# Kernel optimization log

Hardware: AMD Instinct MI355X
Metric: run time of the kernel (lower is better)

The kernel has to match this reference:

```python
import jax, jax.numpy as jnp
import numpy as np

B = 262144
MA = [128, 128]
MB = [128, 128]


def krone_linear(x_a, x_b, wa, wb, ba, bb):
    # slice inputs to each branch's in_features (torch slices the wider branch)
    ia, ib = wa.shape[1], wb.shape[1]
    x_a = x_a[:, :ia]
    x_b = x_b[:, :ib]
    h_a = x_a @ wa.T + ba
    h_b = x_b @ wb.T + bb
    # zero-pad the narrower output so both branches share a width (static shapes)
    oa, ob = wa.shape[0], wb.shape[0]
    if oa > ob:
        h_b = jnp.pad(h_b, ((0, 0), (0, oa - ob)))
    elif ob > oa:
        h_a = jnp.pad(h_a, ((0, 0), (0, ob - oa)))
    return h_a, h_b


def krone_softmax(x_a, x_b, fa, fb):
    x_a = x_a[:, :fa]
    x_b = x_b[:, :fb]
    # vectorized per-row Kronecker product: kron(a, b)[i*fb + j] = a[i]*b[j]
    y = (x_a[:, :, None] * x_b[:, None, :]).reshape(x_a.shape[0], fa * fb)
    return jax.nn.softmax(y, axis=1)


def setup_inputs() -> dict:
    key = jax.random.key(0)
    ks = jax.random.split(key, 13)
    s = 0.1
    inp = {
        "x": jax.random.normal(ks[0], (2, B, 2), dtype=jnp.float32),
        "w1a": jax.random.normal(ks[1], (MA[0], 2), dtype=jnp.float32) * s,
        "w1b": jax.random.normal(ks[2], (MB[0], 2), dtype=jnp.float32) * s,
        "b1a": jax.random.normal(ks[3], (MA[0],), dtype=jnp.float32) * s,
        "b1b": jax.random.normal(ks[4], (MB[0],), dtype=jnp.float32) * s,
        "w2a": jax.random.normal(ks[5], (MA[1], MA[0]), dtype=jnp.float32) * s,
        "w2b": jax.random.normal(ks[6], (MB[1], MB[0]), dtype=jnp.float32) * s,
        "b2a": jax.random.normal(ks[7], (MA[1],), dtype=jnp.float32) * s,
        "b2b": jax.random.normal(ks[8], (MB[1],), dtype=jnp.float32) * s,
        "w3a": jax.random.normal(ks[9], (1, MA[1]), dtype=jnp.float32) * s,
        "w3b": jax.random.normal(ks[10], (3, MB[1]), dtype=jnp.float32) * s,
        "b3a": jax.random.normal(ks[11], (1,), dtype=jnp.float32) * s,
        "b3b": jax.random.normal(ks[12], (3,), dtype=jnp.float32) * s,
    }
    return inp


def reference(x, w1a, w1b, b1a, b1b, w2a, w2b, b2a, b2b, w3a, w3b, b3a, b3b):
    x_a, x_b = x[0], x[1]
    h_a, h_b = krone_linear(x_a, x_b, w1a, w1b, b1a, b1b)
    h_a, h_b = jax.nn.relu(h_a), jax.nn.relu(h_b)
    h_a, h_b = krone_linear(h_a, h_b, w2a, w2b, b2a, b2b)
    h_a, h_b = jax.nn.relu(h_a), jax.nn.relu(h_b)
    h_a, h_b = krone_linear(h_a, h_b, w3a, w3b, b3a, b3b)
    return krone_softmax(h_a, h_b, 1, 3)
```

## Files before the change

kernel.cpp:

```cpp
#include <hip/hip_runtime.h>
#include <hip/hip_bf16.h>


#define BTOT 262144
#define NBLK (BTOT / 512)

typedef __attribute__((ext_vector_type(2))) float floatx2;
typedef __attribute__((ext_vector_type(4))) float floatx4;
typedef __attribute__((ext_vector_type(8))) short bf16x8;
typedef __attribute__((ext_vector_type(4))) int  intx4;

#define OFF_W2  0
#define OFF_W1  65536
#define OFF_B2  68608
#define OFF_W3A 69632
#define OFF_W3B 70144
#define OFF_SA  71680
#define LDS_TOTAL 73728

#if __has_builtin(__builtin_amdgcn_cvt_pk_bf16_f32)
static __device__ __forceinline__ int pack2bf(float lo, float hi) {
    return __builtin_bit_cast(int, __builtin_amdgcn_cvt_pk_bf16_f32(lo, hi));
}
#else
static __device__ __forceinline__ int pack2bf(float lo, float hi) {
    unsigned a = __builtin_bit_cast(unsigned, lo) + 0x8000u;
    unsigned b = __builtin_bit_cast(unsigned, hi) + 0x8000u;
    return (int)__builtin_amdgcn_perm(b, a, 0x07060302u);
}
#endif

#define SEL4(v, i) \
    ((i) == 0 ? (v).x : (i) == 1 ? (v).y : (i) == 2 ? (v).z : (v).w)

static __device__ __forceinline__ floatx4 redcol4(floatx4 v) {
    #pragma unroll
    for (int m = 1; m <= 8; m <<= 1) {
        floatx4 t;
        t.x = __shfl_xor(v.x, m);
        t.y = __shfl_xor(v.y, m);
        t.z = __shfl_xor(v.z, m);
        t.w = __shfl_xor(v.w, m);
        v = v + t;
    }
    return v;
}

static __device__ __forceinline__ floatx4 splat4(float s) {
    return (floatx4){s, s, s, s};
}

#define GEMM_CHUNK(acc, XV, W1P, W2p)                                          \
    {                                                                          \
        const floatx4 Z4 = (floatx4){0.f, 0.f, 0.f, 0.f};                      \
        _Pragma("unroll")                                                      \
        for (int s = 0; s < 4; ++s) {                                          \
            intx4 af[2];                                                       \
            _Pragma("unroll")                                                  \
            for (int j2 = 0; j2 < 4; ++j2) {                                   \
                int kp = s * 16 + quad * 4 + j2;                               \
                floatx2 w0p = (W1P)[kp * 3];                                   \
                floatx2 w1p = (W1P)[kp * 3 + 1];                               \
                floatx2 b1p = (W1P)[kp * 3 + 2];                               \
                _Pragma("unroll")                                              \
                for (int mt = 0; mt < 2; ++mt) {                               \
                    floatx2 xx = (floatx2){(XV)[mt].x, (XV)[mt].x};            \
                    floatx2 xy = (floatx2){(XV)[mt].y, (XV)[mt].y};            \
                    floatx2 h = __builtin_elementwise_fma(xx, w0p,             \
                                  __builtin_elementwise_fma(xy, w1p, b1p));    \
                    h = __builtin_elementwise_max(h, (floatx2){0.f, 0.f});     \
                    af[mt][j2] = pack2bf(h.x, h.y);                            \
                }                                                              \
            }                                                                  \
            _Pragma("unroll")                                                  \
            for (int t = 0; t < 8; ++t) {                                      \
                bf16x8 bfr = (W2p)[(s * 8 + t) * 64 + lane];                   \
                _Pragma("unroll")                                              \
                for (int mt = 0; mt < 2; ++mt) {                               \
                    if (s == 0)                                                \
                        acc[t][mt] = __builtin_amdgcn_mfma_f32_16x16x32_bf16(  \
                            __builtin_bit_cast(bf16x8, af[mt]), bfr, Z4,       \
                            0, 0, 0);                                          \
                    else                                                       \
                        acc[t][mt] = __builtin_amdgcn_mfma_f32_16x16x32_bf16(  \
                            __builtin_bit_cast(bf16x8, af[mt]), bfr,           \
                            acc[t][mt], 0, 0, 0);                              \
                }                                                              \
            }                                                                  \
        }                                                                      \
    }

__global__ __launch_bounds__(512, 4)
void krone_fused(const float* __restrict__ x,
                 const float* __restrict__ w1a, const float* __restrict__ w1b,
                 const float* __restrict__ b1a, const float* __restrict__ b1b,
                 const float* __restrict__ w2a, const float* __restrict__ w2b,
                 const float* __restrict__ b2a, const float* __restrict__ b2b,
                 const float* __restrict__ w3a, const float* __restrict__ w3b,
                 const float* __restrict__ b3a, const float* __restrict__ b3b,
                 float* __restrict__ out) {
    __shared__ __align__(16) unsigned char smem[LDS_TOTAL];

    const int tid  = threadIdx.x;
    const int lane = tid & 63;
    const int wave = tid >> 6;
    const int quad = lane >> 4;
    const int col  = lane & 15;
    const int wbase = blockIdx.x * 512 + wave * 64;

    {
        #pragma unroll
        for (int i = 0; i < 16; ++i) {
            const int path = i >> 3;
            const float4* w2p = (const float4*)(path ? w2b : w2a);
            int n  = (tid & 15) | ((i & 7) << 4);
            int k4 = tid >> 4;
            float4 f = w2p[n * 32 + k4];
            int k = k4 * 4;
            int s = k >> 5;
            int j0 = k & 7;
            int l = ((k & 31) >> 3) * 16 + (n & 15);
            int2 pkd;
            pkd.x = pack2bf(f.x, f.y);
            pkd.y = pack2bf(f.z, f.w);
            *(int2*)(smem + OFF_W2 + path * 32768 +
                     (s * 8 + (n >> 4)) * 1024 + l * 16 + j0 * 2) = pkd;
        }
        if (tid < 128) {
            int p = tid >> 6, kp = tid & 63;
            const float* w1 = p ? w1b : w1a;
            const float* b1 = p ? b1b : b1a;
            float4 w4 = ((const float4*)w1)[kp];
            floatx2* dst = (floatx2*)(smem + OFF_W1) + p * 192 + kp * 3;
            dst[0] = (floatx2){w4.x, w4.z};
            dst[1] = (floatx2){w4.y, w4.w};
            dst[2] = (floatx2){b1[2 * kp], b1[2 * kp + 1]};
            ((float*)(smem + OFF_B2))[tid] = b2a[tid];
            ((float*)(smem + OFF_W3A))[tid] = w3a[tid];
        } else if (tid < 256) {
            ((float*)(smem + OFF_B2))[tid] = b2b[tid - 128];
        }
        if (tid >= 128)
            ((float*)(smem + OFF_W3B))[tid - 128] = w3b[tid - 128];
    }

    const bf16x8*  W2A = (const bf16x8*)(smem + OFF_W2);
    const bf16x8*  W2B = (const bf16x8*)(smem + OFF_W2 + 32768);
    const floatx2* W1A = (const floatx2*)(smem + OFF_W1);
    const floatx2* W1B = W1A + 192;
    const float*   B2A = (const float*)(smem + OFF_B2);
    const float*   B2B = B2A + 128;
    const float*   W3A = (const float*)(smem + OFF_W3A);
    const float*   W3B = (const float*)(smem + OFF_W3B);
    float*         SA  = (float*)(smem + OFF_SA);
    const float2*  xA  = (const float2*)x;
    const float2*  xB  = xA + BTOT;

    const float b3a_ = b3a[0];
    const float b30 = b3b[0], b31 = b3b[1], b32 = b3b[2];

    float2 xv[4];
    #pragma unroll
    for (int c = 0; c < 2; ++c)
        #pragma unroll
        for (int mt = 0; mt < 2; ++mt)
            xv[c * 2 + mt] = xA[wbase + c * 32 + mt * 16 + col];

    __syncthreads();

    #pragma unroll
    for (int c = 0; c < 2; ++c) {
        __builtin_amdgcn_sched_barrier(0);
        floatx4 acc[8][2];
        GEMM_CHUNK(acc, xv + 2 * c, W1A, W2A);
        __builtin_amdgcn_sched_barrier(0);

        floatx4 pa[2] = {(floatx4){0.f,0.f,0.f,0.f}, (floatx4){0.f,0.f,0.f,0.f}};
        #pragma unroll
        for (int t = 0; t < 8; ++t) {
            int n = t * 16 + col;
            floatx4 w4 = splat4(W3A[n]);
            floatx4 b2 = splat4(B2A[n]);
            #pragma unroll
            for (int mt = 0; mt < 2; ++mt) {
                floatx4 h = __builtin_elementwise_max(acc[t][mt] + b2,
                                                      (floatx4){0.f,0.f,0.f,0.f});
                pa[mt] = __builtin_elementwise_fma(w4, h, pa[mt]);
            }
        }
        #pragma unroll
        for (int mt = 0; mt < 2; ++mt) pa[mt] = redcol4(pa[mt]);
        __builtin_amdgcn_sched_barrier(0);

        if (col < 4) {
            #pragma unroll
            for (int mt = 0; mt < 2; ++mt) {
                int sl = mt * 16 + quad * 4 + col;
                SA[wave * 64 + c * 32 + sl] = SEL4(pa[mt], col) + b3a_;
            }
        }
        __builtin_amdgcn_sched_barrier(0);
    }

    #pragma unroll
    for (int c = 0; c < 2; ++c)
        #pragma unroll
        for (int mt = 0; mt < 2; ++mt)
            xv[c * 2 + mt] = xB[wbase + c * 32 + mt * 16 + col];

    #pragma unroll
    for (int c = 0; c < 2; ++c) {
        __builtin_amdgcn_sched_barrier(0);
        floatx4 acc[8][2];
        GEMM_CHUNK(acc, xv + 2 * c, W1B, W2B);
        __builtin_amdgcn_sched_barrier(0);

        #pragma unroll
        for (int mt = 0; mt < 2; ++mt) {
            floatx4 p0 = (floatx4){0.f,0.f,0.f,0.f};
            floatx4 p1 = p0, p2 = p0;
            #pragma unroll
            for (int t = 0; t < 8; ++t) {
                int n = t * 16 + col;
                floatx4 b2 = splat4(B2B[n]);
                floatx4 h = __builtin_elementwise_max(acc[t][mt] + b2,
                                                      (floatx4){0.f,0.f,0.f,0.f});
                p0 = __builtin_elementwise_fma(splat4(W3B[n]),       h, p0);
                p1 = __builtin_elementwise_fma(splat4(W3B[128 + n]), h, p1);
                p2 = __builtin_elementwise_fma(splat4(W3B[256 + n]), h, p2);
            }
            p0 = redcol4(p0); p1 = redcol4(p1); p2 = redcol4(p2);
            if (col < 4) {
                int sl = mt * 16 + quad * 4 + col;
                float t0 = SEL4(p0, col) + b30;
                float t1 = SEL4(p1, col) + b31;
                float t2 = SEL4(p2, col) + b32;
                float sa = SA[wave * 64 + c * 32 + sl];
                float y0 = sa * t0, y1 = sa * t1, y2 = sa * t2;
                float m = fmaxf(y0, fmaxf(y1, y2));
                float e0 = __expf(y0 - m), e1 = __expf(y1 - m), e2 = __expf(y2 - m);
                float rs = 1.f / (e0 + e1 + e2);
                long o = (long)(wbase + c * 32 + sl) * 3;
                out[o]     = e0 * rs;
                out[o + 1] = e1 * rs;
                out[o + 2] = e2 * rs;
            }
        }
        __builtin_amdgcn_sched_barrier(0);
    }
}

extern "C" void kernel_launch(void* const* d_in, const int* in_sizes, int n_in,
                              void* d_out, int out_size, void* d_ws, size_t ws_size,
                              hipStream_t stream) {
    const float* x   = (const float*)d_in[0];
    const float* w1a = (const float*)d_in[1];
    const float* w1b = (const float*)d_in[2];
    const float* b1a = (const float*)d_in[3];
    const float* b1b = (const float*)d_in[4];
    const float* w2a = (const float*)d_in[5];
    const float* w2b = (const float*)d_in[6];
    const float* b2a = (const float*)d_in[7];
    const float* b2b = (const float*)d_in[8];
    const float* w3a = (const float*)d_in[9];
    const float* w3b = (const float*)d_in[10];
    const float* b3a = (const float*)d_in[11];
    const float* b3b = (const float*)d_in[12];
    float* out = (float*)d_out;

    krone_fused<<<NBLK, 512, 0, stream>>>(x, w1a, w1b, b1a, b1b, w2a, w2b,
                                          b2a, b2b, w3a, w3b, b3a, b3b, out);
}
```

Measured before the change: 115.5 us.

## Split N dimension across wave pairs and reduce partial outputs through LDS

Each pair of waves now shares 64 rows, with each wave computing half of the 128 hidden columns over all 64 rows (4 row tiles) instead of one wave doing all columns in two 32-row chunks. Partial layer-3 sums go to LDS, are combined after block barriers, and the softmax is written by one wave per pair. Blocks now cover 256 rows, so the grid doubles. The aim is to reuse each B fragment across 4 row tiles and shorten the per-wave dependency chain. The cost is extra barriers, LDS exchange traffic, a larger LDS footprint, and half the waves sitting idle during the final softmax.

```diff
diff --git a/kernel.cpp b/kernel.cpp
--- a/kernel.cpp
+++ b/kernel.cpp
@@ -3,7 +3,7 @@
 
 
 #define BTOT 262144
-#define NBLK (BTOT / 512)
+#define NBLK (BTOT / 256)
 
 typedef __attribute__((ext_vector_type(2))) float floatx2;
 typedef __attribute__((ext_vector_type(4))) float floatx4;
@@ -15,8 +15,9 @@
 #define OFF_B2  68608
 #define OFF_W3A 69632
 #define OFF_W3B 70144
-#define OFF_SA  71680
-#define LDS_TOTAL 73728
+#define OFF_EXA 71680
+#define OFF_EXB 73728
+#define LDS_TOTAL 79872
 
 #if __has_builtin(__builtin_amdgcn_cvt_pk_bf16_f32)
 static __device__ __forceinline__ int pack2bf(float lo, float hi) {
@@ -50,12 +51,12 @@
     return (floatx4){s, s, s, s};
 }
 
-#define GEMM_CHUNK(acc, XV, W1P, W2p)                                          \
+#define GEMM_PHASE(acc, XV, W1P, W2p)                                          \
     {                                                                          \
         const floatx4 Z4 = (floatx4){0.f, 0.f, 0.f, 0.f};                      \
         _Pragma("unroll")                                                      \
         for (int s = 0; s < 4; ++s) {                                          \
-            intx4 af[2];                                                       \
+            intx4 af[4];                                                       \
             _Pragma("unroll")                                                  \
             for (int j2 = 0; j2 < 4; ++j2) {                                   \
                 int kp = s * 16 + quad * 4 + j2;                               \
@@ -63,7 +64,7 @@
                 floatx2 w1p = (W1P)[kp * 3 + 1];                               \
                 floatx2 b1p = (W1P)[kp * 3 + 2];                               \
                 _Pragma("unroll")                                              \
-                for (int mt = 0; mt < 2; ++mt) {                               \
+                for (int mt = 0; mt < 4; ++mt) {                               \
                     floatx2 xx = (floatx2){(XV)[mt].x, (XV)[mt].x};            \
                     floatx2 xy = (floatx2){(XV)[mt].y, (XV)[mt].y};            \
                     floatx2 h = __builtin_elementwise_fma(xx, w0p,             \
@@ -73,10 +74,10 @@
                 }                                                              \
             }                                                                  \
             _Pragma("unroll")                                                  \
-            for (int t = 0; t < 8; ++t) {                                      \
-                bf16x8 bfr = (W2p)[(s * 8 + t) * 64 + lane];                   \
+            for (int t = 0; t < 4; ++t) {                                      \
+                bf16x8 bfr = (W2p)[(s * 8 + half * 4 + t) * 64 + lane];        \
                 _Pragma("unroll")                                              \
-                for (int mt = 0; mt < 2; ++mt) {                               \
+                for (int mt = 0; mt < 4; ++mt) {                               \
                     if (s == 0)                                                \
                         acc[t][mt] = __builtin_amdgcn_mfma_f32_16x16x32_bf16(  \
                             __builtin_bit_cast(bf16x8, af[mt]), bfr, Z4,       \
@@ -106,7 +107,9 @@
     const int wave = tid >> 6;
     const int quad = lane >> 4;
     const int col  = lane & 15;
-    const int wbase = blockIdx.x * 512 + wave * 64;
+    const int pair = wave >> 1;
+    const int half = wave & 1;
+    const int sbase = blockIdx.x * 256 + pair * 64;
 
     {
         #pragma unroll
@@ -152,101 +155,105 @@
     const float*   B2B = B2A + 128;
     const float*   W3A = (const float*)(smem + OFF_W3A);
     const float*   W3B = (const float*)(smem + OFF_W3B);
-    float*         SA  = (float*)(smem + OFF_SA);
+    float*         EXA = (float*)(smem + OFF_EXA);
+    float*         EXB = (float*)(smem + OFF_EXB);
     const float2*  xA  = (const float2*)x;
     const float2*  xB  = xA + BTOT;
 
     const float b3a_ = b3a[0];
     const float b30 = b3b[0], b31 = b3b[1], b32 = b3b[2];
 
-    float2 xv[4];
+    float2 xa[4], xb[4];
     #pragma unroll
-    for (int c = 0; c < 2; ++c)
-        #pragma unroll
-        for (int mt = 0; mt < 2; ++mt)
-            xv[c * 2 + mt] = xA[wbase + c * 32 + mt * 16 + col];
+    for (int mt = 0; mt < 4; ++mt) {
+        xa[mt] = xA[sbase + mt * 16 + col];
+        xb[mt] = xB[sbase + mt * 16 + col];
+    }
 
     __syncthreads();
 
-    #pragma unroll
-    for (int c = 0; c < 2; ++c) {
-        __builtin_amdgcn_sched_barrier(0);
-        floatx4 acc[8][2];
-        GEMM_CHUNK(acc, xv + 2 * c, W1A, W2A);
-        __builtin_amdgcn_sched_barrier(0);
-
-        floatx4 pa[2] = {(floatx4){0.f,0.f,0.f,0.f}, (floatx4){0.f,0.f,0.f,0.f}};
-        #pragma unroll
-        for (int t = 0; t < 8; ++t) {
-            int n = t * 16 + col;
+    __builtin_amdgcn_sched_barrier(0);
+    floatx4 acc[4][4];
+    GEMM_PHASE(acc, xa, W1A, W2A);
+    __builtin_amdgcn_sched_barrier(0);
+
+    {
+        floatx4 pa[4] = {splat4(0.f), splat4(0.f), splat4(0.f), splat4(0.f)};
+        #pragma unroll
+        for (int t = 0; t < 4; ++t) {
+            int n = (half * 4 + t) * 16 + col;
             floatx4 w4 = splat4(W3A[n]);
             floatx4 b2 = splat4(B2A[n]);
             #pragma unroll
-            for (int mt = 0; mt < 2; ++mt) {
+            for (int mt = 0; mt < 4; ++mt) {
                 floatx4 h = __builtin_elementwise_max(acc[t][mt] + b2,
-                                                      (floatx4){0.f,0.f,0.f,0.f});
+                                                      splat4(0.f));
                 pa[mt] = __builtin_elementwise_fma(w4, h, pa[mt]);
             }
         }
         #pragma unroll
-        for (int mt = 0; mt < 2; ++mt) pa[mt] = redcol4(pa[mt]);
+        for (int mt = 0; mt < 4; ++mt) pa[mt] = redcol4(pa[mt]);
         __builtin_amdgcn_sched_barrier(0);
 
         if (col < 4) {
             #pragma unroll
-            for (int mt = 0; mt < 2; ++mt) {
+            for (int mt = 0; mt < 4; ++mt) {
                 int sl = mt * 16 + quad * 4 + col;
-                SA[wave * 64 + c * 32 + sl] = SEL4(pa[mt], col) + b3a_;
+                EXA[(pair * 64 + sl) * 2 + half] = SEL4(pa[mt], col);
             }
         }
-        __builtin_amdgcn_sched_barrier(0);
-    }
+    }
+    __builtin_amdgcn_sched_barrier(0);
+    __syncthreads();
+
+    float sa;
+    {
+        floatx2 ex = ((const floatx2*)EXA)[pair * 64 + lane];
+        sa = ex.x + ex.y + b3a_;
+    }
+
+    __builtin_amdgcn_sched_barrier(0);
+    GEMM_PHASE(acc, xb, W1B, W2B);
+    __builtin_amdgcn_sched_barrier(0);
 
     #pragma unroll
-    for (int c = 0; c < 2; ++c)
-        #pragma unroll
-        for (int mt = 0; mt < 2; ++mt)
-            xv[c * 2 + mt] = xB[wbase + c * 32 + mt * 16 + col];
-
-    #pragma unroll
-    for (int c = 0; c < 2; ++c) {
-        __builtin_amdgcn_sched_barrier(0);
-        floatx4 acc[8][2];
-        GEMM_CHUNK(acc, xv + 2 * c, W1B, W2B);
-        __builtin_amdgcn_sched_barrier(0);
-
-        #pragma unroll
-        for (int mt = 0; mt < 2; ++mt) {
-            floatx4 p0 = (floatx4){0.f,0.f,0.f,0.f};
-            floatx4 p1 = p0, p2 = p0;
-            #pragma unroll
-            for (int t = 0; t < 8; ++t) {
-                int n = t * 16 + col;
-                floatx4 b2 = splat4(B2B[n]);
-                floatx4 h = __builtin_elementwise_max(acc[t][mt] + b2,
-                                                      (floatx4){0.f,0.f,0.f,0.f});
-                p0 = __builtin_elementwise_fma(splat4(W3B[n]),       h, p0);
-                p1 = __builtin_elementwise_fma(splat4(W3B[128 + n]), h, p1);
-                p2 = __builtin_elementwise_fma(splat4(W3B[256 + n]), h, p2);
-            }
-            p0 = redcol4(p0); p1 = redcol4(p1); p2 = redcol4(p2);
-            if (col < 4) {
-                int sl = mt * 16 + quad * 4 + col;
-                float t0 = SEL4(p0, col) + b30;
-                float t1 = SEL4(p1, col) + b31;
-                float t2 = SEL4(p2, col) + b32;
-                float sa = SA[wave * 64 + c * 32 + sl];
-                float y0 = sa * t0, y1 = sa * t1, y2 = sa * t2;
-                float m = fmaxf(y0, fmaxf(y1, y2));
-                float e0 = __expf(y0 - m), e1 = __expf(y1 - m), e2 = __expf(y2 - m);
-                float rs = 1.f / (e0 + e1 + e2);
-                long o = (long)(wbase + c * 32 + sl) * 3;
-                out[o]     = e0 * rs;
-                out[o + 1] = e1 * rs;
-                out[o + 2] = e2 * rs;
-            }
-        }
-        __builtin_amdgcn_sched_barrier(0);
+    for (int mt = 0; mt < 4; ++mt) {
+        floatx4 p0 = splat4(0.f), p1 = splat4(0.f), p2 = splat4(0.f);
+        #pragma unroll
+        for (int t = 0; t < 4; ++t) {
+            int n = (half * 4 + t) * 16 + col;
+            floatx4 b2 = splat4(B2B[n]);
+            floatx4 h = __builtin_elementwise_max(acc[t][mt] + b2, splat4(0.f));
+            p0 = __builtin_elementwise_fma(splat4(W3B[n]),       h, p0);
+            p1 = __builtin_elementwise_fma(splat4(W3B[128 + n]), h, p1);
+            p2 = __builtin_elementwise_fma(splat4(W3B[256 + n]), h, p2);
+        }
+        p0 = redcol4(p0); p1 = redcol4(p1); p2 = redcol4(p2);
+        if (col < 4) {
+            int sl = mt * 16 + quad * 4 + col;
+            EXB[((0 * 2 + half) * 4 + pair) * 64 + sl] = SEL4(p0, col);
+            EXB[((1 * 2 + half) * 4 + pair) * 64 + sl] = SEL4(p1, col);
+            EXB[((2 * 2 + half) * 4 + pair) * 64 + sl] = SEL4(p2, col);
+        }
+    }
+    __builtin_amdgcn_sched_barrier(0);
+    __syncthreads();
+
+    if (half == 0) {
+        float t0 = EXB[((0 * 2 + 0) * 4 + pair) * 64 + lane]
+                 + EXB[((0 * 2 + 1) * 4 + pair) * 64 + lane] + b30;
+        float t1 = EXB[((1 * 2 + 0) * 4 + pair) * 64 + lane]
+                 + EXB[((1 * 2 + 1) * 4 + pair) * 64 + lane] + b31;
+        float t2 = EXB[((2 * 2 + 0) * 4 + pair) * 64 + lane]
+                 + EXB[((2 * 2 + 1) * 4 + pair) * 64 + lane] + b32;
+        float y0 = sa * t0, y1 = sa * t1, y2 = sa * t2;
+        float m = fmaxf(y0, fmaxf(y1, y2));
+        float e0 = __expf(y0 - m), e1 = __expf(y1 - m), e2 = __expf(y2 - m);
+        float rs = 1.f / (e0 + e1 + e2);
+        long o = (long)(sbase + lane) * 3;
+        out[o]     = e0 * rs;
+        out[o + 1] = e1 * rs;
+        out[o + 2] = e2 * rs;
     }
 }
 
```

After: 132.9 us. 15.1% more time.
